# Performance work log

Measured on AMD Instinct MI355X. Metric: run time of the kernel, lower is better.

The kernel has to match this reference:

```python
import jax, jax.numpy as jnp
import numpy as np

DIM = 1024
HEADS = 16
DIM_HEAD = 64
INNER = HEADS * DIM_HEAD
SCALE = DIM_HEAD ** -0.5
LN_EPS = 1e-5
MASK_VALUE = -np.finfo(np.float32).max


def setup_inputs() -> dict:
    key = jax.random.key(0)
    ks = jax.random.split(key, 3)
    x = jax.random.normal(ks[0], (2, 2048, DIM), dtype=jnp.float32)
    w_qkv = jax.random.normal(ks[1], (DIM, 3 * INNER), dtype=jnp.float32) * (DIM ** -0.5)
    w_out = jax.random.normal(ks[2], (INNER, DIM), dtype=jnp.float32) * (INNER ** -0.5)
    ln_gamma = jnp.ones((DIM,), dtype=jnp.float32)
    ln_beta = jnp.zeros((DIM,), dtype=jnp.float32)
    return {"x": x, "ln_gamma": ln_gamma, "ln_beta": ln_beta, "w_qkv": w_qkv, "w_out": w_out}


def reference(x, ln_gamma, ln_beta, w_qkv, w_out):
    b, n, _ = x.shape
    # LayerNorm
    mu = jnp.mean(x, axis=-1, keepdims=True)
    var = jnp.mean(jnp.square(x - mu), axis=-1, keepdims=True)
    xn = (x - mu) * jax.lax.rsqrt(var + LN_EPS) * ln_gamma + ln_beta
    # QKV projection, split into heads: b n (h d) -> b h n d
    qkv = xn @ w_qkv  # [b, n, 3*inner]
    q, k, v = jnp.split(qkv, 3, axis=-1)
    def to_heads(t):
        return t.reshape(b, n, HEADS, DIM_HEAD).transpose(0, 2, 1, 3)
    q, k, v = to_heads(q), to_heads(k), to_heads(v)
    # scaled scores with diagonal excluded
    dots = jnp.einsum('bhnd,bhmd->bhnm', q, k) * SCALE
    eye = jnp.eye(n, dtype=bool)
    dots = jnp.where(eye, MASK_VALUE, dots)
    attn = jax.nn.softmax(dots, axis=-1)
    out = jnp.einsum('bhnm,bhmd->bhnd', attn, v)
    out = out.transpose(0, 2, 1, 3).reshape(b, n, INNER)
    return out @ w_out
```

## Files before the change

kernel.cpp:

```cpp
#include <hip/hip_runtime.h>


#define DIMM   1024
#define NSEQ   2048
#define BATCH  2
#define HEADS  16
#define DHEAD  64
#define QKVN   3072
#define MROWS  4096

typedef float          f32x4  __attribute__((ext_vector_type(4)));
typedef __bf16         bf16x8 __attribute__((ext_vector_type(8)));
typedef __bf16         bf16x4 __attribute__((ext_vector_type(4)));
typedef unsigned short u16x8  __attribute__((ext_vector_type(8)));
typedef unsigned short u16x4  __attribute__((ext_vector_type(4)));

#define QSCALE (0.125f * 1.4426950408889634f)

#if __has_builtin(__builtin_amdgcn_exp2f)
#define EXP2(x) __builtin_amdgcn_exp2f(x)
#else
#define EXP2(x) exp2f(x)
#endif

__device__ __forceinline__ unsigned short f2bf(float f) {
  unsigned u = __builtin_bit_cast(unsigned, f);
  u += 0x7FFFu + ((u >> 16) & 1u);
  return (unsigned short)(u >> 16);
}
__device__ __forceinline__ bf16x8 as_bf(u16x8 v) { return __builtin_bit_cast(bf16x8, v); }

__device__ __forceinline__ u16x4 cvt4(f32x4 v) {
  bf16x4 b;
  b[0] = (__bf16)v[0]; b[1] = (__bf16)v[1]; b[2] = (__bf16)v[2]; b[3] = (__bf16)v[3];
  return __builtin_bit_cast(u16x4, b);
}

__device__ __forceinline__ void gl_lds16(const unsigned short* g, unsigned short* l) {
  __builtin_amdgcn_global_load_lds(
      (const __attribute__((address_space(1))) unsigned*)g,
      (__attribute__((address_space(3))) unsigned*)l, 16, 0, 0);
}

__device__ __forceinline__ bf16x8 lds_frag(const unsigned short* base, int row, int chunk) {
  return as_bf(*(const u16x8*)&base[row * 64 + ((chunk ^ (row & 7)) << 3)]);
}

__device__ __forceinline__ bf16x8 lds_frag128(const unsigned short* base, int row, int chunk) {
  return as_bf(*(const u16x8*)&base[row * 128 + ((chunk ^ (row & 15)) << 3)]);
}

__device__ __forceinline__ void transpose_tile(
    const float* __restrict__ src, unsigned short* __restrict__ dst,
    int R, int C, int bx, int by, int tid) {
  __shared__ float t[32][33];
  const int rb = by * 32, cb = bx * 32;
  const int r0 = tid >> 5;
  const int c  = tid & 31;
#pragma unroll
  for (int i = 0; i < 4; ++i)
    t[r0 + i * 8][c] = src[(rb + r0 + i * 8) * C + cb + c];
  __syncthreads();
#pragma unroll
  for (int i = 0; i < 4; ++i)
    dst[(cb + r0 + i * 8) * R + rb + c] = f2bf(t[c][r0 + i * 8]);
}

__global__ __launch_bounds__(256) void prep_kernel(
    const float* __restrict__ x, const float* __restrict__ g,
    const float* __restrict__ be, const float* __restrict__ w_qkv,
    const float* __restrict__ w_out, unsigned short* __restrict__ xn,
    unsigned short* __restrict__ wqkvT, unsigned short* __restrict__ woutT) {
  const int bid = blockIdx.x, tid = threadIdx.x;
  if (bid < MROWS) {
    const int row = bid;
    const int wave = tid >> 6, lane = tid & 63;
    const float4 v = *(const float4*)&x[row * DIMM + tid * 4];
    float s  = v.x + v.y + v.z + v.w;
    float s2 = v.x * v.x + v.y * v.y + v.z * v.z + v.w * v.w;
#pragma unroll
    for (int o = 32; o >= 1; o >>= 1) { s += __shfl_xor(s, o); s2 += __shfl_xor(s2, o); }
    __shared__ float ps[4], ps2[4];
    if (lane == 0) { ps[wave] = s; ps2[wave] = s2; }
    __syncthreads();
    s  = ps[0] + ps[1] + ps[2] + ps[3];
    s2 = ps2[0] + ps2[1] + ps2[2] + ps2[3];
    const float mu  = s * (1.0f / DIMM);
    const float var = s2 * (1.0f / DIMM) - mu * mu;
    const float rs  = rsqrtf(var + 1e-5f);
    const float4 gg = *(const float4*)&g[tid * 4];
    const float4 bb = *(const float4*)&be[tid * 4];
    u16x4 o;
    o[0] = f2bf((v.x - mu) * rs * gg.x + bb.x);
    o[1] = f2bf((v.y - mu) * rs * gg.y + bb.y);
    o[2] = f2bf((v.z - mu) * rs * gg.z + bb.z);
    o[3] = f2bf((v.w - mu) * rs * gg.w + bb.w);
    *(u16x4*)&xn[row * DIMM + tid * 4] = o;
  } else {
    const int t = bid - MROWS;
    const int bx = t & 127, by = t >> 7;
    if (bx < QKVN / 32) transpose_tile(w_qkv, wqkvT, DIMM, QKVN, bx, by, tid);
    else                transpose_tile(w_out, woutT, DIMM, DIMM, bx - QKVN / 32, by, tid);
  }
}

__global__ __launch_bounds__(256, 3) void gemm_qkv_kernel(
    const unsigned short* __restrict__ A, const unsigned short* __restrict__ Bt,
    unsigned short* __restrict__ qb, unsigned short* __restrict__ kb,
    unsigned short* __restrict__ vtb) {
  __shared__ __attribute__((aligned(16))) unsigned short As[128 * 64];
  __shared__ __attribute__((aligned(16))) unsigned short Bs[128 * 64];
  const int tid = threadIdx.x;
  const int bm = blockIdx.y, bn = blockIdx.x;
  const int lane = tid & 63, wave = tid >> 6;
  const int l15 = lane & 15, quad = lane >> 4;
  const int wm = wave >> 1, wn = wave & 1;
  const int lrow = lane >> 3;
  const int gcol = ((lane & 7) ^ lrow) << 3;
  const unsigned short* Ab = A  + (bm * 128 + wave * 32 + lrow) * DIMM + gcol;
  const unsigned short* Bb = Bt + (bn * 128 + wave * 32 + lrow) * DIMM + gcol;
  const bool swap = (bn < 16);
  f32x4 acc[4][4] = {};

  for (int k0 = 0; k0 < DIMM; k0 += 64) {
#pragma unroll
    for (int j = 0; j < 4; ++j) {
      gl_lds16(Ab + j * 8 * DIMM + k0, &As[(wave * 32 + j * 8) * 64]);
      gl_lds16(Bb + j * 8 * DIMM + k0, &Bs[(wave * 32 + j * 8) * 64]);
    }
    __syncthreads();
#pragma unroll
    for (int kk = 0; kk < 2; ++kk) {
      bf16x8 af[4], bfr[4];
#pragma unroll
      for (int mi = 0; mi < 4; ++mi) af[mi]  = lds_frag(As, wm * 64 + mi * 16 + l15, kk * 4 + quad);
#pragma unroll
      for (int ni = 0; ni < 4; ++ni) bfr[ni] = lds_frag(Bs, wn * 64 + ni * 16 + l15, kk * 4 + quad);
      if (swap) {
#pragma unroll
        for (int mi = 0; mi < 4; ++mi)
#pragma unroll
          for (int ni = 0; ni < 4; ++ni)
            acc[mi][ni] = __builtin_amdgcn_mfma_f32_16x16x32_bf16(bfr[ni], af[mi], acc[mi][ni], 0, 0, 0);
      } else {
#pragma unroll
        for (int mi = 0; mi < 4; ++mi)
#pragma unroll
          for (int ni = 0; ni < 4; ++ni)
            acc[mi][ni] = __builtin_amdgcn_mfma_f32_16x16x32_bf16(af[mi], bfr[ni], acc[mi][ni], 0, 0, 0);
      }
    }
    __syncthreads();
  }

  if (swap) {
    const int colbase = bn * 128 + wn * 64;
    const int which = colbase >> 10;
    unsigned short* dst = which ? kb : qb;
    const float sc = which ? 1.0f : QSCALE;
#pragma unroll
    for (int mi = 0; mi < 4; ++mi) {
      const int m = bm * 128 + wm * 64 + mi * 16 + l15;
      const int bh0 = (m >> 11) * HEADS;
      const int n = m & 2047;
#pragma unroll
      for (int ni = 0; ni < 4; ++ni) {
        const int wc = (colbase & 1023) + ni * 16 + quad * 4;
        const int h = wc >> 6, dd = wc & 63;
        f32x4 v = acc[mi][ni] * sc;
        *(u16x4*)&dst[((bh0 + h) * NSEQ + n) * DHEAD + dd] = cvt4(v);
      }
    }
  } else {
    const int colbase = bn * 128 + wn * 64 - 2048;
#pragma unroll
    for (int mi = 0; mi < 4; ++mi) {
      const int m0 = bm * 128 + wm * 64 + mi * 16 + quad * 4;
      const int bh0 = (m0 >> 11) * HEADS;
      const int n0 = m0 & 2047;
#pragma unroll
      for (int ni = 0; ni < 4; ++ni) {
        const int vcol = colbase + ni * 16 + l15;
        const int h = vcol >> 6, dd = vcol & 63;
        *(u16x4*)&vtb[((bh0 + h) * DHEAD + dd) * NSEQ + n0] = cvt4(acc[mi][ni]);
      }
    }
  }
}

__global__ __launch_bounds__(512, 4) void attn_kernel(
    const unsigned short* __restrict__ qb, const unsigned short* __restrict__ kb,
    const unsigned short* __restrict__ vtb, unsigned short* __restrict__ attn_out) {
  __shared__ __attribute__((aligned(16))) unsigned short KVs[4][64 * 64];
  __shared__ __attribute__((aligned(16))) unsigned short Ps[8][32][36];
  __shared__ float Lred[4][2][16];
  const int tid = threadIdx.x, wave = tid >> 6, lane = tid & 63;
  const int l15 = lane & 15, quad = lane >> 4;
  const int bh = blockIdx.x, qt = blockIdx.y;
  const int b = bh >> 4, h = bh & 15;
  const int jq = wave & 3;
  const int ikv = wave >> 2;
  const int qbase = qt * 128 + jq * 32;

  bf16x8 aq[2][2];
#pragma unroll
  for (int nt = 0; nt < 2; ++nt) {
    const unsigned short* qrow = qb + (bh * NSEQ + qbase + nt * 16 + l15) * DHEAD;
    aq[nt][0] = as_bf(*(const u16x8*)(qrow + quad * 8));
    aq[nt][1] = as_bf(*(const u16x8*)(qrow + 32 + quad * 8));
  }

  float lsum[2] = {0.f, 0.f};
  f32x4 occ[4][2] = {};

  const int lrow = lane >> 3;
  const int gcol = ((lane & 7) ^ lrow) << 3;
  const unsigned short* Kb = kb  + (bh * NSEQ + wave * 8 + lrow) * DHEAD + gcol;
  const unsigned short* Vb = vtb + (bh * DHEAD + wave * 8 + lrow) * NSEQ + gcol;

  gl_lds16(Kb, &KVs[0][(wave * 8) * 64]);
  gl_lds16(Vb, &KVs[2][(wave * 8) * 64]);

  const int diag_it = qt * 2 + (jq >> 1);
  const bool diag_wave = (ikv == (jq & 1));

  for (int it = 0; it < NSEQ / 64; ++it) {
    const int cur = it & 1;
    __syncthreads();
    if (it < NSEQ / 64 - 1) {
      gl_lds16(Kb + (it + 1) * 64 * DHEAD, &KVs[cur ^ 1][(wave * 8) * 64]);
      gl_lds16(Vb + (it + 1) * 64,         &KVs[2 + (cur ^ 1)][(wave * 8) * 64]);
    }
    bf16x8 ak[2][2];
#pragma unroll
    for (int kk = 0; kk < 2; ++kk)
#pragma unroll
      for (int mt = 0; mt < 2; ++mt)
        ak[kk][mt] = lds_frag(&KVs[cur][0], ikv * 32 + mt * 16 + l15, kk * 4 + quad);
    bf16x8 av[4];
#pragma unroll
    for (int ct = 0; ct < 4; ++ct)
      av[ct] = lds_frag(&KVs[2 + cur][0], ct * 16 + l15, ikv * 4 + quad);

    f32x4 scc[2][2];
#pragma unroll
    for (int mt = 0; mt < 2; ++mt)
#pragma unroll
      for (int nt = 0; nt < 2; ++nt) scc[mt][nt] = (f32x4){-32.f, -32.f, -32.f, -32.f};
    __builtin_amdgcn_s_setprio(1);
#pragma unroll
    for (int kk = 0; kk < 2; ++kk)
#pragma unroll
      for (int mt = 0; mt < 2; ++mt)
#pragma unroll
        for (int nt = 0; nt < 2; ++nt)
          scc[mt][nt] = __builtin_amdgcn_mfma_f32_16x16x32_bf16(ak[kk][mt], aq[nt][kk], scc[mt][nt], 0, 0, 0);
    __builtin_amdgcn_s_setprio(0);

#pragma unroll
    for (int mt = 0; mt < 2; ++mt)
#pragma unroll
      for (int nt = 0; nt < 2; ++nt)
#pragma unroll
        for (int r = 0; r < 4; ++r) scc[mt][nt][r] = EXP2(scc[mt][nt][r]);

    if (it == diag_it && diag_wave) {
#pragma unroll
      for (int nt = 0; nt < 2; ++nt)
#pragma unroll
        for (int r = 0; r < 4; ++r)
          if (quad * 4 + r == l15) scc[nt][nt][r] = 0.f;
    }

#pragma unroll
    for (int nt = 0; nt < 2; ++nt) {
      f32x4 t = scc[0][nt] + scc[1][nt];
      lsum[nt] += (t[0] + t[1]) + (t[2] + t[3]);
    }

#pragma unroll
    for (int mt = 0; mt < 2; ++mt)
#pragma unroll
      for (int nt = 0; nt < 2; ++nt)
        *(u16x4*)&Ps[wave][nt * 16 + l15][mt * 16 + quad * 4] = cvt4(scc[mt][nt]);

    bf16x8 bp[2];
#pragma unroll
    for (int nt = 0; nt < 2; ++nt)
      bp[nt] = as_bf(*(const u16x8*)&Ps[wave][nt * 16 + l15][quad * 8]);

    __builtin_amdgcn_s_setprio(1);
#pragma unroll
    for (int ct = 0; ct < 4; ++ct)
#pragma unroll
      for (int nt = 0; nt < 2; ++nt)
        occ[ct][nt] = __builtin_amdgcn_mfma_f32_16x16x32_bf16(av[ct], bp[nt], occ[ct][nt], 0, 0, 0);
    __builtin_amdgcn_s_setprio(0);
  }

#pragma unroll
  for (int nt = 0; nt < 2; ++nt) {
    lsum[nt] += __shfl_xor(lsum[nt], 16);
    lsum[nt] += __shfl_xor(lsum[nt], 32);
  }

  __syncthreads();
  float* Ored = (float*)&KVs[0][0];
  if (ikv == 1) {
#pragma unroll
    for (int ct = 0; ct < 4; ++ct)
#pragma unroll
      for (int nt = 0; nt < 2; ++nt)
        *(f32x4*)&Ored[((jq * 8 + ct * 2 + nt) * 64 + lane) * 4] = occ[ct][nt];
    if (quad == 0) {
#pragma unroll
      for (int nt = 0; nt < 2; ++nt) Lred[jq][nt][l15] = lsum[nt];
    }
  }
  __syncthreads();
  if (ikv == 0) {
#pragma unroll
    for (int ct = 0; ct < 4; ++ct)
#pragma unroll
      for (int nt = 0; nt < 2; ++nt)
        occ[ct][nt] += *(const f32x4*)&Ored[((jq * 8 + ct * 2 + nt) * 64 + lane) * 4];
#pragma unroll
    for (int nt = 0; nt < 2; ++nt) {
      const float l = lsum[nt] + Lred[jq][nt][l15];
      const float rl = __builtin_amdgcn_rcpf(l);
      const int qg = qbase + nt * 16 + l15;
#pragma unroll
      for (int ct = 0; ct < 4; ++ct) {
        f32x4 ov = occ[ct][nt] * rl;
        *(u16x4*)&attn_out[(b * NSEQ + qg) * DIMM + h * DHEAD + ct * 16 + quad * 4] = cvt4(ov);
      }
    }
  }
}

__global__ __launch_bounds__(256, 2) void gemm_out_kernel(
    const unsigned short* __restrict__ A,
    const unsigned short* __restrict__ Bt,
    float* __restrict__ out) {
  __shared__ __attribute__((aligned(16))) unsigned short As[64 * 128];
  __shared__ __attribute__((aligned(16))) unsigned short Bs[128 * 128];
  const int tid = threadIdx.x;
  const int bm = blockIdx.y, bn = blockIdx.x;
  const int lane = tid & 63, wave = tid >> 6;
  const int l15 = lane & 15, quad = lane >> 4;
  const int wm = wave >> 1, wn = wave & 1;
  const int rl4 = lane >> 4;
  const int cp  = lane & 15;
  const int cx  = cp ^ rl4;
  const int Arow0 = bm * 64 + wave * 16 + rl4;
  const int Brow0 = bn * 128 + wave * 32 + rl4;
  f32x4 acc[2][4] = {};

  for (int it = 0; it < 8; ++it) {
    const int k0 = it * 128;
#pragma unroll
    for (int j = 0; j < 4; ++j)
      gl_lds16(A + (Arow0 + j * 4) * DIMM + k0 + ((cx ^ (j << 2)) << 3),
               &As[(wave * 16 + j * 4) * 128]);
#pragma unroll
    for (int j = 0; j < 8; ++j)
      gl_lds16(Bt + (Brow0 + j * 4) * DIMM + k0 + ((cx ^ ((j & 3) << 2)) << 3),
               &Bs[(wave * 32 + j * 4) * 128]);
    __syncthreads();
#pragma unroll
    for (int kk = 0; kk < 4; ++kk) {
      bf16x8 af[2], bfr[4];
#pragma unroll
      for (int mi = 0; mi < 2; ++mi) af[mi]  = lds_frag128(As, wm * 32 + mi * 16 + l15, kk * 4 + quad);
#pragma unroll
      for (int ni = 0; ni < 4; ++ni) bfr[ni] = lds_frag128(Bs, wn * 64 + ni * 16 + l15, kk * 4 + quad);
#pragma unroll
      for (int mi = 0; mi < 2; ++mi)
#pragma unroll
        for (int ni = 0; ni < 4; ++ni)
          acc[mi][ni] = __builtin_amdgcn_mfma_f32_16x16x32_bf16(bfr[ni], af[mi], acc[mi][ni], 0, 0, 0);
    }
    __syncthreads();
  }
#pragma unroll
  for (int mi = 0; mi < 2; ++mi) {
    const int m = bm * 64 + wm * 32 + mi * 16 + l15;
#pragma unroll
    for (int ni = 0; ni < 4; ++ni) {
      const int col = bn * 128 + wn * 64 + ni * 16 + quad * 4;
      *(f32x4*)&out[m * DIMM + col] = acc[mi][ni];
    }
  }
}

extern "C" void kernel_launch(void* const* d_in, const int* in_sizes, int n_in,
                              void* d_out, int out_size, void* d_ws, size_t ws_size,
                              hipStream_t stream) {
  const float* x     = (const float*)d_in[0];
  const float* gamma = (const float*)d_in[1];
  const float* beta  = (const float*)d_in[2];
  const float* w_qkv = (const float*)d_in[3];
  const float* w_out = (const float*)d_in[4];
  float* out = (float*)d_out;

  char* ws = (char*)d_ws;
  unsigned short* xn    = (unsigned short*)(ws);
  unsigned short* wqkvT = (unsigned short*)(ws + 8388608);
  unsigned short* woutT = (unsigned short*)(ws + 14680064);
  unsigned short* qbuf  = (unsigned short*)(ws + 16777216);
  unsigned short* kbuf  = (unsigned short*)(ws + 25165824);
  unsigned short* vtbuf = (unsigned short*)(ws + 33554432);
  unsigned short* attnb = (unsigned short*)(ws + 41943040);

  prep_kernel<<<MROWS + (QKVN + DIMM) / 32 * (DIMM / 32), 256, 0, stream>>>(
      x, gamma, beta, w_qkv, w_out, xn, wqkvT, woutT);
  gemm_qkv_kernel<<<dim3(24, MROWS / 128), 256, 0, stream>>>(xn, wqkvT, qbuf, kbuf, vtbuf);
  attn_kernel<<<dim3(BATCH * HEADS, NSEQ / 128), 512, 0, stream>>>(qbuf, kbuf, vtbuf, attnb);
  gemm_out_kernel<<<dim3(DIMM / 128, MROWS / 64), 256, 0, stream>>>(attnb, woutT, out);
}
```

Before: 180.8 us.

## Halve attention query tile per block to double grid size and occupancy

Each attention block now handles 64 query rows (16 per wave) instead of 128, so the grid doubles along the sequence axis and per-wave register and LDS state shrinks. Launch bounds rise to 6 blocks per CU to exploit the lower register pressure. The diagonal-mask indexing and the final cross-wave reduction are rewritten for the smaller tile. In exchange, every K/V tile is loaded from global memory twice as often across the grid, and each wave does less MFMA work per LDS fragment read.

```diff
diff --git a/kernel.cpp b/kernel.cpp
--- a/kernel.cpp
+++ b/kernel.cpp
@@ -188,30 +188,29 @@
   }
 }
 
-__global__ __launch_bounds__(512, 4) void attn_kernel(
+__global__ __launch_bounds__(512, 6) void attn_kernel(
     const unsigned short* __restrict__ qb, const unsigned short* __restrict__ kb,
     const unsigned short* __restrict__ vtb, unsigned short* __restrict__ attn_out) {
   __shared__ __attribute__((aligned(16))) unsigned short KVs[4][64 * 64];
-  __shared__ __attribute__((aligned(16))) unsigned short Ps[8][32][36];
-  __shared__ float Lred[4][2][16];
+  __shared__ __attribute__((aligned(16))) unsigned short Ps[8][16][36];
+  __shared__ float Lred[4][16];
   const int tid = threadIdx.x, wave = tid >> 6, lane = tid & 63;
   const int l15 = lane & 15, quad = lane >> 4;
   const int bh = blockIdx.x, qt = blockIdx.y;
   const int b = bh >> 4, h = bh & 15;
   const int jq = wave & 3;
   const int ikv = wave >> 2;
-  const int qbase = qt * 128 + jq * 32;
-
-  bf16x8 aq[2][2];
-#pragma unroll
-  for (int nt = 0; nt < 2; ++nt) {
-    const unsigned short* qrow = qb + (bh * NSEQ + qbase + nt * 16 + l15) * DHEAD;
-    aq[nt][0] = as_bf(*(const u16x8*)(qrow + quad * 8));
-    aq[nt][1] = as_bf(*(const u16x8*)(qrow + 32 + quad * 8));
-  }
-
-  float lsum[2] = {0.f, 0.f};
-  f32x4 occ[4][2] = {};
+  const int qbase = qt * 64 + jq * 16;
+
+  bf16x8 aq[2];
+  {
+    const unsigned short* qrow = qb + (bh * NSEQ + qbase + l15) * DHEAD;
+    aq[0] = as_bf(*(const u16x8*)(qrow + quad * 8));
+    aq[1] = as_bf(*(const u16x8*)(qrow + 32 + quad * 8));
+  }
+
+  float lsum = 0.f;
+  f32x4 occ[4] = {};
 
   const int lrow = lane >> 3;
   const int gcol = ((lane & 7) ^ lrow) << 3;
@@ -221,8 +220,9 @@
   gl_lds16(Kb, &KVs[0][(wave * 8) * 64]);
   gl_lds16(Vb, &KVs[2][(wave * 8) * 64]);
 
-  const int diag_it = qt * 2 + (jq >> 1);
-  const bool diag_wave = (ikv == (jq & 1));
+  const int diag_it = qt;
+  const bool diag_wave = (ikv == (jq >> 1));
+  const int diag_mt = jq & 1;
 
   for (int it = 0; it < NSEQ / 64; ++it) {
     const int cur = it & 1;
@@ -242,98 +242,69 @@
     for (int ct = 0; ct < 4; ++ct)
       av[ct] = lds_frag(&KVs[2 + cur][0], ct * 16 + l15, ikv * 4 + quad);
 
-    f32x4 scc[2][2];
+    f32x4 scc[2];
+#pragma unroll
+    for (int mt = 0; mt < 2; ++mt) scc[mt] = (f32x4){-32.f, -32.f, -32.f, -32.f};
+    __builtin_amdgcn_s_setprio(1);
+#pragma unroll
+    for (int kk = 0; kk < 2; ++kk)
+#pragma unroll
+      for (int mt = 0; mt < 2; ++mt)
+        scc[mt] = __builtin_amdgcn_mfma_f32_16x16x32_bf16(ak[kk][mt], aq[kk], scc[mt], 0, 0, 0);
+    __builtin_amdgcn_s_setprio(0);
+
 #pragma unroll
     for (int mt = 0; mt < 2; ++mt)
 #pragma unroll
-      for (int nt = 0; nt < 2; ++nt) scc[mt][nt] = (f32x4){-32.f, -32.f, -32.f, -32.f};
+      for (int r = 0; r < 4; ++r) scc[mt][r] = EXP2(scc[mt][r]);
+
+    if (it == diag_it && diag_wave) {
+#pragma unroll
+      for (int r = 0; r < 4; ++r)
+        if (quad * 4 + r == l15) scc[diag_mt][r] = 0.f;
+    }
+
+    {
+      f32x4 t = scc[0] + scc[1];
+      lsum += (t[0] + t[1]) + (t[2] + t[3]);
+    }
+
+#pragma unroll
+    for (int mt = 0; mt < 2; ++mt)
+      *(u16x4*)&Ps[wave][l15][mt * 16 + quad * 4] = cvt4(scc[mt]);
+
+    bf16x8 bp = as_bf(*(const u16x8*)&Ps[wave][l15][quad * 8]);
+
     __builtin_amdgcn_s_setprio(1);
 #pragma unroll
-    for (int kk = 0; kk < 2; ++kk)
-#pragma unroll
-      for (int mt = 0; mt < 2; ++mt)
-#pragma unroll
-        for (int nt = 0; nt < 2; ++nt)
-          scc[mt][nt] = __builtin_amdgcn_mfma_f32_16x16x32_bf16(ak[kk][mt], aq[nt][kk], scc[mt][nt], 0, 0, 0);
+    for (int ct = 0; ct < 4; ++ct)
+      occ[ct] = __builtin_amdgcn_mfma_f32_16x16x32_bf16(av[ct], bp, occ[ct], 0, 0, 0);
     __builtin_amdgcn_s_setprio(0);
-
-#pragma unroll
-    for (int mt = 0; mt < 2; ++mt)
-#pragma unroll
-      for (int nt = 0; nt < 2; ++nt)
-#pragma unroll
-        for (int r = 0; r < 4; ++r) scc[mt][nt][r] = EXP2(scc[mt][nt][r]);
-
-    if (it == diag_it && diag_wave) {
-#pragma unroll
-      for (int nt = 0; nt < 2; ++nt)
-#pragma unroll
-        for (int r = 0; r < 4; ++r)
-          if (quad * 4 + r == l15) scc[nt][nt][r] = 0.f;
-    }
-
-#pragma unroll
-    for (int nt = 0; nt < 2; ++nt) {
-      f32x4 t = scc[0][nt] + scc[1][nt];
-      lsum[nt] += (t[0] + t[1]) + (t[2] + t[3]);
-    }
-
-#pragma unroll
-    for (int mt = 0; mt < 2; ++mt)
-#pragma unroll
-      for (int nt = 0; nt < 2; ++nt)
-        *(u16x4*)&Ps[wave][nt * 16 + l15][mt * 16 + quad * 4] = cvt4(scc[mt][nt]);
-
-    bf16x8 bp[2];
-#pragma unroll
-    for (int nt = 0; nt < 2; ++nt)
-      bp[nt] = as_bf(*(const u16x8*)&Ps[wave][nt * 16 + l15][quad * 8]);
-
-    __builtin_amdgcn_s_setprio(1);
-#pragma unroll
-    for (int ct = 0; ct < 4; ++ct)
-#pragma unroll
-      for (int nt = 0; nt < 2; ++nt)
-        occ[ct][nt] = __builtin_amdgcn_mfma_f32_16x16x32_bf16(av[ct], bp[nt], occ[ct][nt], 0, 0, 0);
-    __builtin_amdgcn_s_setprio(0);
-  }
-
-#pragma unroll
-  for (int nt = 0; nt < 2; ++nt) {
-    lsum[nt] += __shfl_xor(lsum[nt], 16);
-    lsum[nt] += __shfl_xor(lsum[nt], 32);
-  }
+  }
+
+  lsum += __shfl_xor(lsum, 16);
+  lsum += __shfl_xor(lsum, 32);
 
   __syncthreads();
   float* Ored = (float*)&KVs[0][0];
   if (ikv == 1) {
 #pragma unroll
     for (int ct = 0; ct < 4; ++ct)
-#pragma unroll
-      for (int nt = 0; nt < 2; ++nt)
-        *(f32x4*)&Ored[((jq * 8 + ct * 2 + nt) * 64 + lane) * 4] = occ[ct][nt];
-    if (quad == 0) {
-#pragma unroll
-      for (int nt = 0; nt < 2; ++nt) Lred[jq][nt][l15] = lsum[nt];
-    }
+      *(f32x4*)&Ored[((jq * 4 + ct) * 64 + lane) * 4] = occ[ct];
+    if (quad == 0) Lred[jq][l15] = lsum;
   }
   __syncthreads();
   if (ikv == 0) {
 #pragma unroll
     for (int ct = 0; ct < 4; ++ct)
-#pragma unroll
-      for (int nt = 0; nt < 2; ++nt)
-        occ[ct][nt] += *(const f32x4*)&Ored[((jq * 8 + ct * 2 + nt) * 64 + lane) * 4];
-#pragma unroll
-    for (int nt = 0; nt < 2; ++nt) {
-      const float l = lsum[nt] + Lred[jq][nt][l15];
-      const float rl = __builtin_amdgcn_rcpf(l);
-      const int qg = qbase + nt * 16 + l15;
-#pragma unroll
-      for (int ct = 0; ct < 4; ++ct) {
-        f32x4 ov = occ[ct][nt] * rl;
-        *(u16x4*)&attn_out[(b * NSEQ + qg) * DIMM + h * DHEAD + ct * 16 + quad * 4] = cvt4(ov);
-      }
+      occ[ct] += *(const f32x4*)&Ored[((jq * 4 + ct) * 64 + lane) * 4];
+    const float l = lsum + Lred[jq][l15];
+    const float rl = __builtin_amdgcn_rcpf(l);
+    const int qg = qbase + l15;
+#pragma unroll
+    for (int ct = 0; ct < 4; ++ct) {
+      f32x4 ov = occ[ct] * rl;
+      *(u16x4*)&attn_out[(b * NSEQ + qg) * DIMM + h * DHEAD + ct * 16 + quad * 4] = cvt4(ov);
     }
   }
 }
@@ -415,6 +386,6 @@
   prep_kernel<<<MROWS + (QKVN + DIMM) / 32 * (DIMM / 32), 256, 0, stream>>>(
       x, gamma, beta, w_qkv, w_out, xn, wqkvT, woutT);
   gemm_qkv_kernel<<<dim3(24, MROWS / 128), 256, 0, stream>>>(xn, wqkvT, qbuf, kbuf, vtbuf);
-  attn_kernel<<<dim3(BATCH * HEADS, NSEQ / 128), 512, 0, stream>>>(qbuf, kbuf, vtbuf, attnb);
+  attn_kernel<<<dim3(BATCH * HEADS, NSEQ / 64), 512, 0, stream>>>(qbuf, kbuf, vtbuf, attnb);
   gemm_out_kernel<<<dim3(DIMM / 128, MROWS / 64), 256, 0, stream>>>(attnb, woutT, out);
 }
```

New measurement: 195.0 us. 1.08x slower.
